# Kernel optimization log

Hardware: AMD Instinct MI355X
Metric: run time of the kernel (lower is better)

Reference implementation:

```python
import jax, jax.numpy as jnp
import numpy as np

B, N, C, H = 8, 4096, 768, 32
D = C // H  # head_dim = 24
EPS = 1e-12


def _l2norm(t):
    # F.normalize(dim=-1): t / max(||t||_2, eps)
    n = jnp.sqrt(jnp.sum(t * t, axis=-1, keepdims=True))
    return t / jnp.maximum(n, EPS)


def setup_inputs() -> dict:
    key = jax.random.key(0)
    ks = jax.random.split(key, 6)
    s_in = 1.0 / np.sqrt(C)
    return {
        "x": jax.random.normal(ks[0], (B, N, C), dtype=jnp.float32),
        "W_qkv": jax.random.uniform(ks[1], (C, 3 * C), jnp.float32, -s_in, s_in),
        "b_qkv": jax.random.uniform(ks[2], (3 * C,), jnp.float32, -s_in, s_in),
        "temperature": jnp.ones((H, 1, 1), dtype=jnp.float32),
        "W_proj": jax.random.uniform(ks[3], (C, C), jnp.float32, -s_in, s_in),
        "b_proj": jax.random.uniform(ks[4], (C,), jnp.float32, -s_in, s_in),
    }


def reference(x, W_qkv, b_qkv, temperature, W_proj, b_proj):
    b, n, c = x.shape
    qkv = x @ W_qkv + b_qkv                                  # (B,N,3C)
    qkv = qkv.reshape(b, n, 3, H, D).transpose(2, 0, 3, 1, 4)  # (3,B,H,N,D)
    q, k, v = qkv[0], qkv[1], qkv[2]                         # (B,H,N,D)
    q = jnp.swapaxes(q, -1, -2)                              # (B,H,D,N)
    k = jnp.swapaxes(k, -1, -2)
    v = jnp.swapaxes(v, -1, -2)
    q = _l2norm(q)                                           # normalize over N
    k = _l2norm(k)
    attn = jnp.einsum('bhdn,bhen->bhde', q, k) * temperature  # (B,H,D,D)
    attn = jax.nn.softmax(attn, axis=-1)
    y = jnp.einsum('bhde,bhen->bhdn', attn, v)               # (B,H,D,N)
    # Faithful to torch: (1,B,H,D,N).transpose(1,2).reshape(B,N,C)
    # == (H,B,D,N) flattened row-major into (B,N,C)
    y = jnp.transpose(y, (1, 0, 2, 3)).reshape(b, n, c)
    return y @ W_proj + b_proj
```

## Files before the change

kernel.cpp:

```cpp
#include <hip/hip_runtime.h>
#include <hip/hip_bf16.h>


#define DEVI __device__ __forceinline__

typedef __attribute__((ext_vector_type(8))) short bf16x8;
typedef __attribute__((ext_vector_type(4))) float f32x4;
typedef unsigned int u32;
typedef unsigned short u16;

DEVI u16 f2bf(float f) {
  union { float f; u32 u; } x; x.f = f;
  u32 r = x.u + 0x7FFFu + ((x.u >> 16) & 1u);
  return (u16)(r >> 16);
}

DEVI void gload_lds16(const void* g, void* l) {
  __builtin_amdgcn_global_load_lds((__attribute__((address_space(1))) void*)g,
                                   (__attribute__((address_space(3))) void*)l, 16, 0, 0);
}

__global__ __launch_bounds__(256) void cvt_kernel(const float* __restrict__ in,
                                                  u16* __restrict__ out, int n8) {
  int i = blockIdx.x * 256 + threadIdx.x;
  if (i >= n8) return;
  long o = (long)i * 8;
  float4 a = *(const float4*)(in + o);
  float4 b = *(const float4*)(in + o + 4);
  uint4 v;
  v.x = f2bf(a.x) | ((u32)f2bf(a.y) << 16);
  v.y = f2bf(a.z) | ((u32)f2bf(a.w) << 16);
  v.z = f2bf(b.x) | ((u32)f2bf(b.y) << 16);
  v.w = f2bf(b.z) | ((u32)f2bf(b.w) << 16);
  *(uint4*)(out + o) = v;
}

__global__ __launch_bounds__(256) void transpose_cvt(const float* __restrict__ W,
                                                     u16* __restrict__ Wt, int K, int N) {
  __shared__ float tile[32][33];
  int n0 = blockIdx.x * 32, k0 = blockIdx.y * 32;
  int tx = threadIdx.x, ty = threadIdx.y;
  #pragma unroll
  for (int i = 0; i < 4; ++i)
    tile[ty + 8 * i][tx] = W[(long)(k0 + ty + 8 * i) * N + n0 + tx];
  __syncthreads();
  #pragma unroll
  for (int i = 0; i < 4; ++i)
    Wt[(long)(n0 + ty + 8 * i) * K + k0 + tx] = f2bf(tile[tx][ty + 8 * i]);
}

#define STAGE_T(ktile, slot)                                                   \
  { gload_lds16(Ag + soffA + (ktile) * 32, lds + (slot) * 8192 + sdst);        \
    _Pragma("unroll") for (int j_ = 0; j_ < 2; ++j_)                           \
      gload_lds16(Bg + soffB[j_] + (ktile) * 32,                               \
                  lds + 24576 + (slot) * 16384 + j_ * 8192 + sdst); }

template<int NT, int BF16_OUT>
__global__ __launch_bounds__(512, 4) void gemm2b_kernel(
    const u16* __restrict__ A, const u16* __restrict__ Bt,
    const float* __restrict__ bias, void* __restrict__ Cout,
    int M, int N) {
  constexpr int K = NT * 32;
  __shared__ __attribute__((aligned(128))) char lds[73728];

  int nbx = N >> 8;
  int nwg = gridDim.x;
  int bid = blockIdx.x;
  bid = (bid & 7) * (nwg >> 3) + (bid >> 3);
  int bx = bid % nbx, by = bid / nbx;

  int t = threadIdx.x;
  int w = t >> 6, l = t & 63;
  int wr = w >> 2, wc = w & 3;
  int l16 = l & 15, l4 = l >> 4;

  int cbb = (l4 * 16) ^ ((l16 & 8) << 2);
  int pA0 = (wr * 64 + l16) * 64 + cbb;
  int pB0 = (wc * 64 + l16) * 64 + cbb;

  int pa = t * 16;
  int la = pa ^ (((pa >> 9) & 1) << 5);
  int soffA = (la >> 6) * K + ((la & 63) >> 1);
  int soffB[2];
  #pragma unroll
  for (int j = 0; j < 2; ++j) {
    int p = (j * 512 + t) * 16;
    int lb = p ^ (((p >> 9) & 1) << 5);
    soffB[j] = (lb >> 6) * K + ((lb & 63) >> 1);
  }

  const u16* Ag = A + (long)by * 128 * K;
  const u16* Bg = Bt + (long)bx * 256 * K;
  int sdst = w * 1024;

  f32x4 acc[4][4] = {};

  STAGE_T(0, 0);
  STAGE_T(1, 1);

  #pragma unroll
  for (int kt = 0; kt < NT; ++kt) {
    int rs = kt % 3;
    if (kt + 2 < NT) {
      STAGE_T(kt + 2, (kt + 2) % 3);
      asm volatile("s_waitcnt vmcnt(6)" ::: "memory");
    } else if (kt + 2 == NT) {
      asm volatile("s_waitcnt vmcnt(3)" ::: "memory");
    } else {
      asm volatile("s_waitcnt vmcnt(0)" ::: "memory");
    }
    __builtin_amdgcn_sched_barrier(0);
    __builtin_amdgcn_s_barrier();
    __builtin_amdgcn_sched_barrier(0);

    bf16x8 aF[4], bF[4];
    #pragma unroll
    for (int mi = 0; mi < 4; ++mi)
      aF[mi] = *(const bf16x8*)(lds + rs * 8192 + mi * 1024 + pA0);
    #pragma unroll
    for (int n = 0; n < 4; ++n)
      bF[n] = *(const bf16x8*)(lds + 24576 + rs * 16384 + n * 1024 + pB0);

    __builtin_amdgcn_s_setprio(1);
    #pragma unroll
    for (int mi = 0; mi < 4; ++mi)
      #pragma unroll
      for (int n = 0; n < 4; ++n)
        acc[mi][n] = __builtin_amdgcn_mfma_f32_16x16x32_bf16(aF[mi], bF[n], acc[mi][n], 0, 0, 0);
    __builtin_amdgcn_s_setprio(0);
    __builtin_amdgcn_s_barrier();
    __builtin_amdgcn_sched_barrier(0);
  }

  #pragma unroll
  for (int mi = 0; mi < 4; ++mi) {
    int row0 = by * 128 + wr * 64 + mi * 16 + l4 * 4;
    #pragma unroll
    for (int n = 0; n < 4; ++n) {
      int col = bx * 256 + wc * 64 + n * 16 + l16;
      float bv = bias[col];
      #pragma unroll
      for (int j = 0; j < 4; ++j) {
        long idx = (long)(row0 + j) * N + col;
        float v = acc[mi][n][j] + bv;
        if (BF16_OUT) ((u16*)Cout)[idx] = f2bf(v);
        else          __builtin_nontemporal_store(v, (float*)Cout + idx);
      }
    }
  }
}

#define PFQK(nc, rq, rk)                                                       \
  { long cb = (long)(nc) * 589824;                                             \
    _Pragma("unroll") for (int i = 0; i < 3; ++i) {                            \
      rq[i] = *(const uint4*)(qbase + cb + offI[i]);                           \
      rk[i] = *(const uint4*)(kbase + cb + offI[i]); } }

#define WRQK(rq, rk)                                                           \
  { _Pragma("unroll") for (int i = 0; i < 3; ++i) {                            \
      const u32* pq = (const u32*)&rq[i];                                      \
      const u32* pk = (const u32*)&rk[i];                                      \
      _Pragma("unroll") for (int j = 0; j < 4; ++j) {                          \
        int d = sI[i] * 8 + 2 * j;                                             \
        qt[d][nI[i]] = (u16)pq[j]; qt[d + 1][nI[i]] = (u16)(pq[j] >> 16);      \
        kt[d][nI[i]] = (u16)pk[j]; kt[d + 1][nI[i]] = (u16)(pk[j] >> 16); } } }

#define GRAM8                                                                  \
  { _Pragma("unroll") for (int ks = 0; ks < 8; ++ks) {                         \
      int koff = ks * 32 + l4 * 8;                                             \
      bf16x8 qa = *(const bf16x8*)&qt[fm * 16 + l16][koff];                    \
      bf16x8 qb = *(const bf16x8*)&qt[fn * 16 + l16][koff];                    \
      bf16x8 ka = *(const bf16x8*)&kt[fm * 16 + l16][koff];                    \
      bf16x8 kb = *(const bf16x8*)&kt[fn * 16 + l16][koff];                    \
      accG = __builtin_amdgcn_mfma_f32_16x16x32_bf16(qa, kb, accG, 0, 0, 0);   \
      accQ = __builtin_amdgcn_mfma_f32_16x16x32_bf16(qa, qb, accQ, 0, 0, 0);   \
      accK = __builtin_amdgcn_mfma_f32_16x16x32_bf16(ka, kb, accK, 0, 0, 0); } }

#define PFV(nc, rv)                                                            \
  { long cb = (long)(nc) * 589824;                                             \
    _Pragma("unroll") for (int i = 0; i < 3; ++i)                              \
      rv[i] = *(const uint4*)(vbase + cb + offI[i]); }

#define WRV(rv)                                                                \
  { _Pragma("unroll") for (int i = 0; i < 3; ++i)                              \
      *(uint4*)&vl[nI[i]][sI[i] * 8] = rv[i]; }

#define PV_STORE(nc)                                                           \
  { int n0 = (nc) * 256;                                                       \
    f32x4 z = {};                                                              \
    _Pragma("unroll") for (int fnn = 0; fnn < 4; ++fnn) {                      \
      int ncol = w * 64 + fnn * 16 + l16;                                      \
      bf16x8 bv = *(const bf16x8*)&vl[ncol][l4 * 8];                           \
      f32x4 y0 = __builtin_amdgcn_mfma_f32_16x16x32_bf16(af0, bv, z, 0, 0, 0); \
      f32x4 y1 = __builtin_amdgcn_mfma_f32_16x16x32_bf16(af1, bv, z, 0, 0, 0); \
      int gn = n0 + ncol;                                                      \
      _Pragma("unroll") for (int j = 0; j < 4; ++j) {                          \
        int d0 = l4 * 4 + j;                                                   \
        ybase[(long)d0 * 4096 + gn] = f2bf(y0[j]);                             \
        int d1 = 16 + d0;                                                      \
        if (d1 < 24) ybase[(long)d1 * 4096 + gn] = f2bf(y1[j]); } } }

__global__ __launch_bounds__(256) void attn_kernel(const u16* __restrict__ qkv,
                                                   const float* __restrict__ temperature,
                                                   u16* __restrict__ yout) {
  __shared__ u16 qt[32][272];
  __shared__ u16 kt[32][272];
  __shared__ u16 vl[256][40];
  __shared__ u16 attnb[32][40];
  __shared__ float Gs[32][33];
  __shared__ float sq[32];
  __shared__ float sk[32];

  int bid = blockIdx.x;
  int b = bid >> 5, h = bid & 31;
  int t = threadIdx.x;
  int w = t >> 6, l = t & 63;
  int l16 = l & 15, l4 = l >> 4;
  int fm = w >> 1, fn = w & 1;

  for (int i = t; i < 32 * 272; i += 256) { qt[0][i] = 0; kt[0][i] = 0; }
  for (int i = t; i < 256 * 40; i += 256) vl[0][i] = 0;
  for (int i = t; i < 32 * 40; i += 256) attnb[0][i] = 0;

  int nI[3], sI[3], offI[3];
  #pragma unroll
  for (int i = 0; i < 3; ++i) {
    int idx = t + 256 * i;
    nI[i] = idx / 3; sI[i] = idx % 3;
    offI[i] = nI[i] * 2304 + sI[i] * 8;
  }

  f32x4 accG = {}, accQ = {}, accK = {};
  const u16* qbase = qkv + (long)b * 4096 * 2304 + h * 24;
  const u16* kbase = qbase + 768;
  const u16* vbase = qbase + 1536;

  uint4 rqA[3], rkA[3], rqB[3], rkB[3];
  PFQK(0, rqA, rkA);
  PFQK(1, rqB, rkB);
  __syncthreads();

  for (int nc = 0; nc < 16; nc += 2) {
    WRQK(rqA, rkA);
    __syncthreads();
    if (nc + 2 < 16) PFQK(nc + 2, rqA, rkA);
    GRAM8;
    __syncthreads();
    WRQK(rqB, rkB);
    __syncthreads();
    if (nc + 3 < 16) PFQK(nc + 3, rqB, rkB);
    GRAM8;
    __syncthreads();
  }

  #pragma unroll
  for (int j = 0; j < 4; ++j) Gs[fm * 16 + l4 * 4 + j][fn * 16 + l16] = accG[j];
  if (fm == fn) {
    #pragma unroll
    for (int j = 0; j < 4; ++j)
      if (l4 * 4 + j == l16) { sq[fm * 16 + l16] = accQ[j]; sk[fm * 16 + l16] = accK[j]; }
  }
  __syncthreads();

  if (t < 24) {
    float nq = fmaxf(sqrtf(fmaxf(sq[t], 0.f)), 1e-12f);
    float tmp = temperature[h];
    float p[24]; float mx = -1e30f;
    #pragma unroll
    for (int e = 0; e < 24; ++e) {
      float nk = fmaxf(sqrtf(fmaxf(sk[e], 0.f)), 1e-12f);
      float a = Gs[t][e] / (nq * nk) * tmp;
      p[e] = a; mx = fmaxf(mx, a);
    }
    float s = 0.f;
    #pragma unroll
    for (int e = 0; e < 24; ++e) { p[e] = __expf(p[e] - mx); s += p[e]; }
    float inv = 1.f / s;
    #pragma unroll
    for (int e = 0; e < 24; ++e) attnb[t][e] = f2bf(p[e] * inv);
  }

  uint4 rvA[3], rvB[3];
  PFV(0, rvA);
  PFV(1, rvB);
  __syncthreads();

  bf16x8 af0 = *(const bf16x8*)&attnb[l16][l4 * 8];
  bf16x8 af1 = *(const bf16x8*)&attnb[16 + l16][l4 * 8];
  u16* ybase = yout + (long)(h * 8 + b) * 24 * 4096;

  for (int nc = 0; nc < 16; nc += 2) {
    WRV(rvA);
    __syncthreads();
    if (nc + 2 < 16) PFV(nc + 2, rvA);
    PV_STORE(nc);
    __syncthreads();
    WRV(rvB);
    __syncthreads();
    if (nc + 3 < 16) PFV(nc + 3, rvB);
    PV_STORE(nc + 1);
    __syncthreads();
  }
}

extern "C" void kernel_launch(void* const* d_in, const int* in_sizes, int n_in,
                              void* d_out, int out_size, void* d_ws, size_t ws_size,
                              hipStream_t stream) {
  const float* x     = (const float*)d_in[0];
  const float* Wqkv  = (const float*)d_in[1];
  const float* bqkv  = (const float*)d_in[2];
  const float* temp  = (const float*)d_in[3];
  const float* Wproj = (const float*)d_in[4];
  const float* bproj = (const float*)d_in[5];
  float* out = (float*)d_out;

  char* ws = (char*)d_ws;
  u16* xb  = (u16*)(ws);
  u16* wqt = (u16*)(ws + 50331648);
  u16* wpt = (u16*)(ws + 53870592);
  u16* qkv = (u16*)(ws + 55050240);
  u16* y   = xb;

  cvt_kernel<<<12288, 256, 0, stream>>>(x, xb, 3145728);
  transpose_cvt<<<dim3(72, 24), dim3(32, 8), 0, stream>>>(Wqkv, wqt, 768, 2304);
  transpose_cvt<<<dim3(24, 24), dim3(32, 8), 0, stream>>>(Wproj, wpt, 768, 768);
  gemm2b_kernel<24, 1><<<2304, 512, 0, stream>>>(xb, wqt, bqkv, qkv, 32768, 2304);
  attn_kernel<<<256, 256, 0, stream>>>(qkv, temp, y);
  gemm2b_kernel<24, 0><<<768, 512, 0, stream>>>(y, wpt, bproj, out, 32768, 768);
}
```

Baseline: 309.6 us.

## Fuse fp32-to-bf16 x conversion into QKV GEMM and split attention over N

Removes the separate cvt_kernel. The QKV GEMM now stages fp32 x tiles directly into LDS and converts them to bf16 in registers with v_cvt_pk_bf16_f32, saving a full write and re-read of the activation. The attention kernel doubles to 512 threads, with two groups each handling half of the N range. Their partial Gram matrices and norms are summed through LDS, and the V prefetch is moved earlier. This trades extra LDS traffic and in-loop conversion work in the GEMM for fewer passes over memory and more parallelism per attention block.

```diff
diff --git a/kernel.cpp b/kernel.cpp
--- a/kernel.cpp
+++ b/kernel.cpp
@@ -6,6 +6,7 @@
 
 typedef __attribute__((ext_vector_type(8))) short bf16x8;
 typedef __attribute__((ext_vector_type(4))) float f32x4;
+typedef __attribute__((ext_vector_type(4))) unsigned int u32x4;
 typedef unsigned int u32;
 typedef unsigned short u16;
 
@@ -15,24 +16,15 @@
   return (u16)(r >> 16);
 }
 
+DEVI u32 cvtpk(float a, float b) {
+  u32 r;
+  asm("v_cvt_pk_bf16_f32 %0, %1, %2" : "=v"(r) : "v"(a), "v"(b));
+  return r;
+}
+
 DEVI void gload_lds16(const void* g, void* l) {
   __builtin_amdgcn_global_load_lds((__attribute__((address_space(1))) void*)g,
                                    (__attribute__((address_space(3))) void*)l, 16, 0, 0);
-}
-
-__global__ __launch_bounds__(256) void cvt_kernel(const float* __restrict__ in,
-                                                  u16* __restrict__ out, int n8) {
-  int i = blockIdx.x * 256 + threadIdx.x;
-  if (i >= n8) return;
-  long o = (long)i * 8;
-  float4 a = *(const float4*)(in + o);
-  float4 b = *(const float4*)(in + o + 4);
-  uint4 v;
-  v.x = f2bf(a.x) | ((u32)f2bf(a.y) << 16);
-  v.y = f2bf(a.z) | ((u32)f2bf(a.w) << 16);
-  v.z = f2bf(b.x) | ((u32)f2bf(b.y) << 16);
-  v.w = f2bf(b.z) | ((u32)f2bf(b.w) << 16);
-  *(uint4*)(out + o) = v;
 }
 
 __global__ __launch_bounds__(256) void transpose_cvt(const float* __restrict__ W,
@@ -49,16 +41,125 @@
     Wt[(long)(n0 + ty + 8 * i) * K + k0 + tx] = f2bf(tile[tx][ty + 8 * i]);
 }
 
+template<int NT>
+__global__ __launch_bounds__(512, 4) void gemm_k1_kernel(
+    const float* __restrict__ X, const u16* __restrict__ Bt,
+    const float* __restrict__ bias, u16* __restrict__ Cout, int N) {
+  constexpr int K = NT * 32;
+  __shared__ __attribute__((aligned(128))) char lds[65536];
+
+  int nbx = N >> 8;
+  int nwg = gridDim.x;
+  int bid = blockIdx.x;
+  bid = (bid & 7) * (nwg >> 3) + (bid >> 3);
+  int bx = bid % nbx, by = bid / nbx;
+
+  int t = threadIdx.x;
+  int w = t >> 6, l = t & 63;
+  int wr = w >> 2, wc = w & 3;
+  int l16 = l & 15, l4 = l >> 4;
+
+  int rowA = wr * 64 + l16;
+  int xA = (l16 & 7) << 4;
+  int a0 = rowA * 128 + ((l4 * 32) ^ xA);
+  int a1 = rowA * 128 + ((l4 * 32 + 16) ^ xA);
+  int cbb = (l4 * 16) ^ ((l16 & 8) << 2);
+  int pB0 = 32768 + (wc * 64 + l16) * 64 + cbb;
+
+  int soffA[2], soffB[2];
+  #pragma unroll
+  for (int j = 0; j < 2; ++j) {
+    int p = (j * 512 + t) * 16;
+    int pa = p ^ (((p >> 7) & 7) << 4);
+    soffA[j] = (pa >> 7) * K + ((pa & 127) >> 2);
+    int pb = p ^ (((p >> 9) & 1) << 5);
+    soffB[j] = (pb >> 6) * K + ((pb & 63) >> 1);
+  }
+
+  const float* Ag = X + (long)by * 128 * K;
+  const u16* Bg = Bt + (long)bx * 256 * K;
+  int sdst = w * 1024;
+
+  f32x4 acc[4][4] = {};
+
+  #pragma unroll
+  for (int j = 0; j < 2; ++j) {
+    gload_lds16(Ag + soffA[j], lds + j * 8192 + sdst);
+    gload_lds16(Bg + soffB[j], lds + 32768 + j * 8192 + sdst);
+  }
+
+  #pragma unroll 2
+  for (int kt = 0; kt < NT; ++kt) {
+    int s = kt & 1;
+    if (kt + 1 < NT) {
+      #pragma unroll
+      for (int j = 0; j < 2; ++j) {
+        gload_lds16(Ag + soffA[j] + (kt + 1) * 32,
+                    lds + (s ^ 1) * 16384 + j * 8192 + sdst);
+        gload_lds16(Bg + soffB[j] + (kt + 1) * 32,
+                    lds + 32768 + (s ^ 1) * 16384 + j * 8192 + sdst);
+      }
+      asm volatile("s_waitcnt vmcnt(4)" ::: "memory");
+    } else {
+      asm volatile("s_waitcnt vmcnt(0)" ::: "memory");
+    }
+    __builtin_amdgcn_sched_barrier(0);
+    __builtin_amdgcn_s_barrier();
+    __builtin_amdgcn_sched_barrier(0);
+
+    bf16x8 aF[4], bF[4];
+    #pragma unroll
+    for (int mi = 0; mi < 4; ++mi) {
+      f32x4 u = *(const f32x4*)(lds + s * 16384 + mi * 2048 + a0);
+      f32x4 v = *(const f32x4*)(lds + s * 16384 + mi * 2048 + a1);
+      union { u32x4 u4; bf16x8 v8; } cc;
+      cc.u4[0] = cvtpk(u[0], u[1]);
+      cc.u4[1] = cvtpk(u[2], u[3]);
+      cc.u4[2] = cvtpk(v[0], v[1]);
+      cc.u4[3] = cvtpk(v[2], v[3]);
+      aF[mi] = cc.v8;
+    }
+    #pragma unroll
+    for (int n = 0; n < 4; ++n)
+      bF[n] = *(const bf16x8*)(lds + s * 16384 + n * 1024 + pB0);
+
+    __builtin_amdgcn_s_setprio(1);
+    #pragma unroll
+    for (int mi = 0; mi < 4; ++mi)
+      #pragma unroll
+      for (int n = 0; n < 4; ++n)
+        acc[mi][n] = __builtin_amdgcn_mfma_f32_16x16x32_bf16(aF[mi], bF[n], acc[mi][n], 0, 0, 0);
+    __builtin_amdgcn_s_setprio(0);
+    __builtin_amdgcn_s_barrier();
+    __builtin_amdgcn_sched_barrier(0);
+  }
+
+  #pragma unroll
+  for (int mi = 0; mi < 4; ++mi) {
+    int row0 = by * 128 + wr * 64 + mi * 16 + l4 * 4;
+    #pragma unroll
+    for (int n = 0; n < 4; ++n) {
+      int col = bx * 256 + wc * 64 + n * 16 + l16;
+      float bv = bias[col];
+      #pragma unroll
+      for (int j = 0; j < 4; ++j) {
+        long idx = (long)(row0 + j) * N + col;
+        Cout[idx] = f2bf(acc[mi][n][j] + bv);
+      }
+    }
+  }
+}
+
 #define STAGE_T(ktile, slot)                                                   \
   { gload_lds16(Ag + soffA + (ktile) * 32, lds + (slot) * 8192 + sdst);        \
     _Pragma("unroll") for (int j_ = 0; j_ < 2; ++j_)                           \
       gload_lds16(Bg + soffB[j_] + (ktile) * 32,                               \
                   lds + 24576 + (slot) * 16384 + j_ * 8192 + sdst); }
 
-template<int NT, int BF16_OUT>
+template<int NT>
 __global__ __launch_bounds__(512, 4) void gemm2b_kernel(
     const u16* __restrict__ A, const u16* __restrict__ Bt,
-    const float* __restrict__ bias, void* __restrict__ Cout,
+    const float* __restrict__ bias, float* __restrict__ Cout,
     int M, int N) {
   constexpr int K = NT * 32;
   __shared__ __attribute__((aligned(128))) char lds[73728];
@@ -142,9 +243,7 @@
       #pragma unroll
       for (int j = 0; j < 4; ++j) {
         long idx = (long)(row0 + j) * N + col;
-        float v = acc[mi][n][j] + bv;
-        if (BF16_OUT) ((u16*)Cout)[idx] = f2bf(v);
-        else          __builtin_nontemporal_store(v, (float*)Cout + idx);
+        __builtin_nontemporal_store(acc[mi][n][j] + bv, Cout + idx);
       }
     }
   }
@@ -162,16 +261,16 @@
       const u32* pk = (const u32*)&rk[i];                                      \
       _Pragma("unroll") for (int j = 0; j < 4; ++j) {                          \
         int d = sI[i] * 8 + 2 * j;                                             \
-        qt[d][nI[i]] = (u16)pq[j]; qt[d + 1][nI[i]] = (u16)(pq[j] >> 16);      \
-        kt[d][nI[i]] = (u16)pk[j]; kt[d + 1][nI[i]] = (u16)(pk[j] >> 16); } } }
+        qtg[d][nI[i]] = (u16)pq[j]; qtg[d + 1][nI[i]] = (u16)(pq[j] >> 16);    \
+        ktg[d][nI[i]] = (u16)pk[j]; ktg[d + 1][nI[i]] = (u16)(pk[j] >> 16); } } }
 
 #define GRAM8                                                                  \
   { _Pragma("unroll") for (int ks = 0; ks < 8; ++ks) {                         \
       int koff = ks * 32 + l4 * 8;                                             \
-      bf16x8 qa = *(const bf16x8*)&qt[fm * 16 + l16][koff];                    \
-      bf16x8 qb = *(const bf16x8*)&qt[fn * 16 + l16][koff];                    \
-      bf16x8 ka = *(const bf16x8*)&kt[fm * 16 + l16][koff];                    \
-      bf16x8 kb = *(const bf16x8*)&kt[fn * 16 + l16][koff];                    \
+      bf16x8 qa = *(const bf16x8*)&qtg[fm * 16 + l16][koff];                   \
+      bf16x8 qb = *(const bf16x8*)&qtg[fn * 16 + l16][koff];                   \
+      bf16x8 ka = *(const bf16x8*)&ktg[fm * 16 + l16][koff];                   \
+      bf16x8 kb = *(const bf16x8*)&ktg[fn * 16 + l16][koff];                   \
       accG = __builtin_amdgcn_mfma_f32_16x16x32_bf16(qa, kb, accG, 0, 0, 0);   \
       accQ = __builtin_amdgcn_mfma_f32_16x16x32_bf16(qa, qb, accQ, 0, 0, 0);   \
       accK = __builtin_amdgcn_mfma_f32_16x16x32_bf16(ka, kb, accK, 0, 0, 0); } }
@@ -183,14 +282,14 @@
 
 #define WRV(rv)                                                                \
   { _Pragma("unroll") for (int i = 0; i < 3; ++i)                              \
-      *(uint4*)&vl[nI[i]][sI[i] * 8] = rv[i]; }
+      *(uint4*)&vlg[nI[i]][sI[i] * 8] = rv[i]; }
 
 #define PV_STORE(nc)                                                           \
   { int n0 = (nc) * 256;                                                       \
     f32x4 z = {};                                                              \
     _Pragma("unroll") for (int fnn = 0; fnn < 4; ++fnn) {                      \
-      int ncol = w * 64 + fnn * 16 + l16;                                      \
-      bf16x8 bv = *(const bf16x8*)&vl[ncol][l4 * 8];                           \
+      int ncol = wg * 64 + fnn * 16 + l16;                                     \
+      bf16x8 bv = *(const bf16x8*)&vlg[ncol][l4 * 8];                          \
       f32x4 y0 = __builtin_amdgcn_mfma_f32_16x16x32_bf16(af0, bv, z, 0, 0, 0); \
       f32x4 y1 = __builtin_amdgcn_mfma_f32_16x16x32_bf16(af1, bv, z, 0, 0, 0); \
       int gn = n0 + ncol;                                                      \
@@ -200,32 +299,38 @@
         int d1 = 16 + d0;                                                      \
         if (d1 < 24) ybase[(long)d1 * 4096 + gn] = f2bf(y1[j]); } } }
 
-__global__ __launch_bounds__(256) void attn_kernel(const u16* __restrict__ qkv,
+__global__ __launch_bounds__(512) void attn_kernel(const u16* __restrict__ qkv,
                                                    const float* __restrict__ temperature,
                                                    u16* __restrict__ yout) {
-  __shared__ u16 qt[32][272];
-  __shared__ u16 kt[32][272];
-  __shared__ u16 vl[256][40];
+  __shared__ u16 qt[2][32][280];
+  __shared__ u16 kt[2][32][280];
+  __shared__ u16 vl[2][256][40];
   __shared__ u16 attnb[32][40];
-  __shared__ float Gs[32][33];
-  __shared__ float sq[32];
-  __shared__ float sk[32];
+  __shared__ float Gs[2][32][33];
+  __shared__ float sq[2][32];
+  __shared__ float sk[2][32];
 
   int bid = blockIdx.x;
   int b = bid >> 5, h = bid & 31;
   int t = threadIdx.x;
   int w = t >> 6, l = t & 63;
+  int g = t >> 8, lt = t & 255;
+  int wg = w & 3;
   int l16 = l & 15, l4 = l >> 4;
-  int fm = w >> 1, fn = w & 1;
-
-  for (int i = t; i < 32 * 272; i += 256) { qt[0][i] = 0; kt[0][i] = 0; }
-  for (int i = t; i < 256 * 40; i += 256) vl[0][i] = 0;
-  for (int i = t; i < 32 * 40; i += 256) attnb[0][i] = 0;
+  int fm = wg >> 1, fn = wg & 1;
+
+  for (int i = t; i < 2 * 32 * 280; i += 512) { ((u16*)qt)[i] = 0; ((u16*)kt)[i] = 0; }
+  for (int i = t; i < 2 * 256 * 40; i += 512) ((u16*)vl)[i] = 0;
+  for (int i = t; i < 32 * 40; i += 512) ((u16*)attnb)[i] = 0;
+
+  u16 (*qtg)[280] = qt[g];
+  u16 (*ktg)[280] = kt[g];
+  u16 (*vlg)[40] = vl[g];
 
   int nI[3], sI[3], offI[3];
   #pragma unroll
   for (int i = 0; i < 3; ++i) {
-    int idx = t + 256 * i;
+    int idx = lt + 256 * i;
     nI[i] = idx / 3; sI[i] = idx % 3;
     offI[i] = nI[i] * 2304 + sI[i] * 8;
   }
@@ -234,42 +339,47 @@
   const u16* qbase = qkv + (long)b * 4096 * 2304 + h * 24;
   const u16* kbase = qbase + 768;
   const u16* vbase = qbase + 1536;
+  int c0 = g * 8;
 
   uint4 rqA[3], rkA[3], rqB[3], rkB[3];
-  PFQK(0, rqA, rkA);
-  PFQK(1, rqB, rkB);
+  PFQK(c0 + 0, rqA, rkA);
+  PFQK(c0 + 1, rqB, rkB);
   __syncthreads();
 
-  for (int nc = 0; nc < 16; nc += 2) {
+  for (int c = 0; c < 8; c += 2) {
     WRQK(rqA, rkA);
     __syncthreads();
-    if (nc + 2 < 16) PFQK(nc + 2, rqA, rkA);
+    if (c + 2 < 8) PFQK(c0 + c + 2, rqA, rkA);
     GRAM8;
     __syncthreads();
     WRQK(rqB, rkB);
     __syncthreads();
-    if (nc + 3 < 16) PFQK(nc + 3, rqB, rkB);
+    if (c + 3 < 8) PFQK(c0 + c + 3, rqB, rkB);
     GRAM8;
     __syncthreads();
   }
 
   #pragma unroll
-  for (int j = 0; j < 4; ++j) Gs[fm * 16 + l4 * 4 + j][fn * 16 + l16] = accG[j];
+  for (int j = 0; j < 4; ++j) Gs[g][fm * 16 + l4 * 4 + j][fn * 16 + l16] = accG[j];
   if (fm == fn) {
     #pragma unroll
     for (int j = 0; j < 4; ++j)
-      if (l4 * 4 + j == l16) { sq[fm * 16 + l16] = accQ[j]; sk[fm * 16 + l16] = accK[j]; }
-  }
+      if (l4 * 4 + j == l16) { sq[g][fm * 16 + l16] = accQ[j]; sk[g][fm * 16 + l16] = accK[j]; }
+  }
+
+  uint4 rvA[3], rvB[3];
+  PFV(c0 + 0, rvA);
+  PFV(c0 + 1, rvB);
   __syncthreads();
 
   if (t < 24) {
-    float nq = fmaxf(sqrtf(fmaxf(sq[t], 0.f)), 1e-12f);
+    float nq = fmaxf(sqrtf(fmaxf(sq[0][t] + sq[1][t], 0.f)), 1e-12f);
     float tmp = temperature[h];
     float p[24]; float mx = -1e30f;
     #pragma unroll
     for (int e = 0; e < 24; ++e) {
-      float nk = fmaxf(sqrtf(fmaxf(sk[e], 0.f)), 1e-12f);
-      float a = Gs[t][e] / (nq * nk) * tmp;
+      float nk = fmaxf(sqrtf(fmaxf(sk[0][e] + sk[1][e], 0.f)), 1e-12f);
+      float a = (Gs[0][t][e] + Gs[1][t][e]) / (nq * nk) * tmp;
       p[e] = a; mx = fmaxf(mx, a);
     }
     float s = 0.f;
@@ -279,26 +389,22 @@
     #pragma unroll
     for (int e = 0; e < 24; ++e) attnb[t][e] = f2bf(p[e] * inv);
   }
-
-  uint4 rvA[3], rvB[3];
-  PFV(0, rvA);
-  PFV(1, rvB);
   __syncthreads();
 
   bf16x8 af0 = *(const bf16x8*)&attnb[l16][l4 * 8];
   bf16x8 af1 = *(const bf16x8*)&attnb[16 + l16][l4 * 8];
   u16* ybase = yout + (long)(h * 8 + b) * 24 * 4096;
 
-  for (int nc = 0; nc < 16; nc += 2) {
+  for (int c = 0; c < 8; c += 2) {
     WRV(rvA);
     __syncthreads();
-    if (nc + 2 < 16) PFV(nc + 2, rvA);
-    PV_STORE(nc);
+    if (c + 2 < 8) PFV(c0 + c + 2, rvA);
+    PV_STORE(c0 + c);
     __syncthreads();
     WRV(rvB);
     __syncthreads();
-    if (nc + 3 < 16) PFV(nc + 3, rvB);
-    PV_STORE(nc + 1);
+    if (c + 3 < 8) PFV(c0 + c + 3, rvB);
+    PV_STORE(c0 + c + 1);
     __syncthreads();
   }
 }
@@ -315,16 +421,14 @@
   float* out = (float*)d_out;
 
   char* ws = (char*)d_ws;
-  u16* xb  = (u16*)(ws);
+  u16* y   = (u16*)(ws);
   u16* wqt = (u16*)(ws + 50331648);
   u16* wpt = (u16*)(ws + 53870592);
   u16* qkv = (u16*)(ws + 55050240);
-  u16* y   = xb;
-
-  cvt_kernel<<<12288, 256, 0, stream>>>(x, xb, 3145728);
+
   transpose_cvt<<<dim3(72, 24), dim3(32, 8), 0, stream>>>(Wqkv, wqt, 768, 2304);
   transpose_cvt<<<dim3(24, 24), dim3(32, 8), 0, stream>>>(Wproj, wpt, 768, 768);
-  gemm2b_kernel<24, 1><<<2304, 512, 0, stream>>>(xb, wqt, bqkv, qkv, 32768, 2304);
-  attn_kernel<<<256, 256, 0, stream>>>(qkv, temp, y);
-  gemm2b_kernel<24, 0><<<768, 512, 0, stream>>>(y, wpt, bproj, out, 32768, 768);
-}
+  gemm_k1_kernel<24><<<2304, 512, 0, stream>>>(x, wqt, bqkv, qkv, 2304);
+  attn_kernel<<<256, 512, 0, stream>>>(qkv, temp, y);
+  gemm2b_kernel<24><<<768, 512, 0, stream>>>(y, wpt, bproj, out, 32768, 768);
+}
```

Result: slower. 346.0 us (+11.8%).

## Split attention kernel into split-N gram, softmax, and parallel PV kernels

Applied to the files above, without the earlier changes.

The single 256-block attention kernel is replaced by three kernels. A gram kernel splits the N dimension four ways (1024 blocks) and writes partial Gram and norm matrices to workspace. A small softmax kernel reduces the partials and writes the bf16 attention matrix. A PV kernel runs 4096 blocks, one per 256-column chunk. The aim is to fill the GPU, which the old 256-block launch underused. The cost is two extra launches and workspace round-trips, and the workspace buffers are reused across stages (the gram buffer aliases xb and y, attnb aliases wqt).

```diff
diff --git a/kernel.cpp b/kernel.cpp
--- a/kernel.cpp
+++ b/kernel.cpp
@@ -176,51 +176,20 @@
       accQ = __builtin_amdgcn_mfma_f32_16x16x32_bf16(qa, qb, accQ, 0, 0, 0);   \
       accK = __builtin_amdgcn_mfma_f32_16x16x32_bf16(ka, kb, accK, 0, 0, 0); } }
 
-#define PFV(nc, rv)                                                            \
-  { long cb = (long)(nc) * 589824;                                             \
-    _Pragma("unroll") for (int i = 0; i < 3; ++i)                              \
-      rv[i] = *(const uint4*)(vbase + cb + offI[i]); }
-
-#define WRV(rv)                                                                \
-  { _Pragma("unroll") for (int i = 0; i < 3; ++i)                              \
-      *(uint4*)&vl[nI[i]][sI[i] * 8] = rv[i]; }
-
-#define PV_STORE(nc)                                                           \
-  { int n0 = (nc) * 256;                                                       \
-    f32x4 z = {};                                                              \
-    _Pragma("unroll") for (int fnn = 0; fnn < 4; ++fnn) {                      \
-      int ncol = w * 64 + fnn * 16 + l16;                                      \
-      bf16x8 bv = *(const bf16x8*)&vl[ncol][l4 * 8];                           \
-      f32x4 y0 = __builtin_amdgcn_mfma_f32_16x16x32_bf16(af0, bv, z, 0, 0, 0); \
-      f32x4 y1 = __builtin_amdgcn_mfma_f32_16x16x32_bf16(af1, bv, z, 0, 0, 0); \
-      int gn = n0 + ncol;                                                      \
-      _Pragma("unroll") for (int j = 0; j < 4; ++j) {                          \
-        int d0 = l4 * 4 + j;                                                   \
-        ybase[(long)d0 * 4096 + gn] = f2bf(y0[j]);                             \
-        int d1 = 16 + d0;                                                      \
-        if (d1 < 24) ybase[(long)d1 * 4096 + gn] = f2bf(y1[j]); } } }
-
-__global__ __launch_bounds__(256) void attn_kernel(const u16* __restrict__ qkv,
-                                                   const float* __restrict__ temperature,
-                                                   u16* __restrict__ yout) {
-  __shared__ u16 qt[32][272];
-  __shared__ u16 kt[32][272];
-  __shared__ u16 vl[256][40];
-  __shared__ u16 attnb[32][40];
-  __shared__ float Gs[32][33];
-  __shared__ float sq[32];
-  __shared__ float sk[32];
+__global__ __launch_bounds__(256) void gram_kernel(const u16* __restrict__ qkv,
+                                                   float* __restrict__ gram) {
+  __shared__ u16 qt[32][280];
+  __shared__ u16 kt[32][280];
 
   int bid = blockIdx.x;
-  int b = bid >> 5, h = bid & 31;
+  int bh = bid >> 2, s = bid & 3;
+  int b = bh >> 5, h = bh & 31;
   int t = threadIdx.x;
   int w = t >> 6, l = t & 63;
   int l16 = l & 15, l4 = l >> 4;
   int fm = w >> 1, fn = w & 1;
 
-  for (int i = t; i < 32 * 272; i += 256) { qt[0][i] = 0; kt[0][i] = 0; }
-  for (int i = t; i < 256 * 40; i += 256) vl[0][i] = 0;
-  for (int i = t; i < 32 * 40; i += 256) attnb[0][i] = 0;
+  for (int i = t; i < 32 * 280; i += 256) { qt[0][i] = 0; kt[0][i] = 0; }
 
   int nI[3], sI[3], offI[3];
   #pragma unroll
@@ -233,73 +202,124 @@
   f32x4 accG = {}, accQ = {}, accK = {};
   const u16* qbase = qkv + (long)b * 4096 * 2304 + h * 24;
   const u16* kbase = qbase + 768;
-  const u16* vbase = qbase + 1536;
-
-  uint4 rqA[3], rkA[3], rqB[3], rkB[3];
-  PFQK(0, rqA, rkA);
-  PFQK(1, rqB, rkB);
+  int c0 = s * 4;
+
+  uint4 rq[3], rk[3];
+  PFQK(c0, rq, rk);
   __syncthreads();
 
-  for (int nc = 0; nc < 16; nc += 2) {
-    WRQK(rqA, rkA);
+  #pragma unroll
+  for (int c = 0; c < 4; ++c) {
+    WRQK(rq, rk);
     __syncthreads();
-    if (nc + 2 < 16) PFQK(nc + 2, rqA, rkA);
+    if (c + 1 < 4) PFQK(c0 + c + 1, rq, rk);
     GRAM8;
     __syncthreads();
-    WRQK(rqB, rkB);
-    __syncthreads();
-    if (nc + 3 < 16) PFQK(nc + 3, rqB, rkB);
-    GRAM8;
-    __syncthreads();
-  }
-
-  #pragma unroll
-  for (int j = 0; j < 4; ++j) Gs[fm * 16 + l4 * 4 + j][fn * 16 + l16] = accG[j];
-  if (fm == fn) {
-    #pragma unroll
-    for (int j = 0; j < 4; ++j)
-      if (l4 * 4 + j == l16) { sq[fm * 16 + l16] = accQ[j]; sk[fm * 16 + l16] = accK[j]; }
+  }
+
+  float* gb = gram + (long)(bh * 4 + s) * 3072;
+  int row = fm * 16 + l4 * 4, col = fn * 16 + l16;
+  #pragma unroll
+  for (int j = 0; j < 4; ++j) {
+    gb[(row + j) * 32 + col] = accG[j];
+    gb[1024 + (row + j) * 32 + col] = accQ[j];
+    gb[2048 + (row + j) * 32 + col] = accK[j];
+  }
+}
+
+__global__ __launch_bounds__(32) void softmax_kernel(const float* __restrict__ gram,
+                                                     const float* __restrict__ temperature,
+                                                     u16* __restrict__ attnb) {
+  int bh = blockIdx.x;
+  int h = bh & 31;
+  int d = threadIdx.x;
+  u16* ab = attnb + bh * 1024;
+  if (d < 24) {
+    const float* gb = gram + (long)bh * 12288;
+    float nq2 = 0.f, row[24], nk2[24];
+    #pragma unroll
+    for (int e = 0; e < 24; ++e) { row[e] = 0.f; nk2[e] = 0.f; }
+    #pragma unroll
+    for (int s = 0; s < 4; ++s) {
+      const float* gs = gb + s * 3072;
+      nq2 += gs[1024 + d * 33];
+      #pragma unroll
+      for (int e = 0; e < 24; ++e) {
+        row[e] += gs[d * 32 + e];
+        nk2[e] += gs[2048 + e * 33];
+      }
+    }
+    float nq = fmaxf(sqrtf(fmaxf(nq2, 0.f)), 1e-12f);
+    float tmp = temperature[h];
+    float mx = -1e30f;
+    #pragma unroll
+    for (int e = 0; e < 24; ++e) {
+      float nk = fmaxf(sqrtf(fmaxf(nk2[e], 0.f)), 1e-12f);
+      row[e] = row[e] / (nq * nk) * tmp;
+      mx = fmaxf(mx, row[e]);
+    }
+    float ssum = 0.f;
+    #pragma unroll
+    for (int e = 0; e < 24; ++e) { row[e] = __expf(row[e] - mx); ssum += row[e]; }
+    float inv = 1.f / ssum;
+    #pragma unroll
+    for (int e = 0; e < 24; ++e) ab[d * 32 + e] = f2bf(row[e] * inv);
+    #pragma unroll
+    for (int e = 24; e < 32; ++e) ab[d * 32 + e] = 0;
+  } else {
+    #pragma unroll
+    for (int e = 0; e < 32; ++e) ab[d * 32 + e] = 0;
+  }
+}
+
+__global__ __launch_bounds__(256) void pv_kernel(const u16* __restrict__ qkv,
+                                                 const u16* __restrict__ attnb,
+                                                 u16* __restrict__ yout) {
+  __shared__ u16 vl[256][40];
+  int bid = blockIdx.x;
+  int bh = bid >> 4, c = bid & 15;
+  int b = bh >> 5, h = bh & 31;
+  int t = threadIdx.x;
+  int w = t >> 6, l = t & 63;
+  int l16 = l & 15, l4 = l >> 4;
+
+  for (int i = t; i < 5120; i += 256) ((u32*)vl)[i] = 0;
+
+  const u16* ab = attnb + bh * 1024;
+  bf16x8 af0 = *(const bf16x8*)(ab + l16 * 32 + l4 * 8);
+  bf16x8 af1 = *(const bf16x8*)(ab + (16 + l16) * 32 + l4 * 8);
+
+  const u16* vbase = qkv + (long)b * 4096 * 2304 + h * 24 + 1536;
+  uint4 rv[3];
+  int nI[3], sI[3];
+  #pragma unroll
+  for (int i = 0; i < 3; ++i) {
+    int idx = t + 256 * i;
+    nI[i] = idx / 3; sI[i] = idx % 3;
+    rv[i] = *(const uint4*)(vbase + (long)c * 589824 + nI[i] * 2304 + sI[i] * 8);
   }
   __syncthreads();
-
-  if (t < 24) {
-    float nq = fmaxf(sqrtf(fmaxf(sq[t], 0.f)), 1e-12f);
-    float tmp = temperature[h];
-    float p[24]; float mx = -1e30f;
-    #pragma unroll
-    for (int e = 0; e < 24; ++e) {
-      float nk = fmaxf(sqrtf(fmaxf(sk[e], 0.f)), 1e-12f);
-      float a = Gs[t][e] / (nq * nk) * tmp;
-      p[e] = a; mx = fmaxf(mx, a);
-    }
-    float s = 0.f;
-    #pragma unroll
-    for (int e = 0; e < 24; ++e) { p[e] = __expf(p[e] - mx); s += p[e]; }
-    float inv = 1.f / s;
-    #pragma unroll
-    for (int e = 0; e < 24; ++e) attnb[t][e] = f2bf(p[e] * inv);
-  }
-
-  uint4 rvA[3], rvB[3];
-  PFV(0, rvA);
-  PFV(1, rvB);
+  #pragma unroll
+  for (int i = 0; i < 3; ++i) *(uint4*)&vl[nI[i]][sI[i] * 8] = rv[i];
   __syncthreads();
 
-  bf16x8 af0 = *(const bf16x8*)&attnb[l16][l4 * 8];
-  bf16x8 af1 = *(const bf16x8*)&attnb[16 + l16][l4 * 8];
   u16* ybase = yout + (long)(h * 8 + b) * 24 * 4096;
-
-  for (int nc = 0; nc < 16; nc += 2) {
-    WRV(rvA);
-    __syncthreads();
-    if (nc + 2 < 16) PFV(nc + 2, rvA);
-    PV_STORE(nc);
-    __syncthreads();
-    WRV(rvB);
-    __syncthreads();
-    if (nc + 3 < 16) PFV(nc + 3, rvB);
-    PV_STORE(nc + 1);
-    __syncthreads();
+  int n0 = c * 256;
+  f32x4 z = {};
+  #pragma unroll
+  for (int fnn = 0; fnn < 4; ++fnn) {
+    int ncol = w * 64 + fnn * 16 + l16;
+    bf16x8 bv = *(const bf16x8*)&vl[ncol][l4 * 8];
+    f32x4 y0 = __builtin_amdgcn_mfma_f32_16x16x32_bf16(af0, bv, z, 0, 0, 0);
+    f32x4 y1 = __builtin_amdgcn_mfma_f32_16x16x32_bf16(af1, bv, z, 0, 0, 0);
+    int gn = n0 + ncol;
+    #pragma unroll
+    for (int j = 0; j < 4; ++j) {
+      int d0 = l4 * 4 + j;
+      ybase[(long)d0 * 4096 + gn] = f2bf(y0[j]);
+      int d1 = 16 + d0;
+      if (d1 < 24) ybase[(long)d1 * 4096 + gn] = f2bf(y1[j]);
+    }
   }
 }
 
@@ -315,16 +335,20 @@
   float* out = (float*)d_out;
 
   char* ws = (char*)d_ws;
-  u16* xb  = (u16*)(ws);
-  u16* wqt = (u16*)(ws + 50331648);
-  u16* wpt = (u16*)(ws + 53870592);
-  u16* qkv = (u16*)(ws + 55050240);
-  u16* y   = xb;
+  u16*   xb    = (u16*)(ws);
+  float* gram  = (float*)(ws);
+  u16*   y     = (u16*)(ws);
+  u16*   wqt   = (u16*)(ws + 50331648);
+  u16*   attnb = (u16*)(ws + 50331648);
+  u16*   wpt   = (u16*)(ws + 53870592);
+  u16*   qkv   = (u16*)(ws + 55050240);
 
   cvt_kernel<<<12288, 256, 0, stream>>>(x, xb, 3145728);
   transpose_cvt<<<dim3(72, 24), dim3(32, 8), 0, stream>>>(Wqkv, wqt, 768, 2304);
   transpose_cvt<<<dim3(24, 24), dim3(32, 8), 0, stream>>>(Wproj, wpt, 768, 768);
   gemm2b_kernel<24, 1><<<2304, 512, 0, stream>>>(xb, wqt, bqkv, qkv, 32768, 2304);
-  attn_kernel<<<256, 256, 0, stream>>>(qkv, temp, y);
+  gram_kernel<<<1024, 256, 0, stream>>>(qkv, gram);
+  softmax_kernel<<<256, 32, 0, stream>>>(gram, temp, attnb);
+  pv_kernel<<<4096, 256, 0, stream>>>(qkv, attnb, y);
   gemm2b_kernel<24, 0><<<768, 512, 0, stream>>>(y, wpt, bproj, out, 32768, 768);
 }
```

Measured after the change: 299.0 us. -3.4%, faster.
